# Kernel optimization log

Measured on AMD Instinct MI355X. Metric: run time of the kernel, lower is better.

## Reference

```python
import jax, jax.numpy as jnp
import numpy as np

B, N, D, H = 4, 256, 32, 512

def setup_inputs() -> dict:
    key = jax.random.key(0)
    ks = jax.random.split(key, 6)
    z = jax.random.normal(ks[0], (B, N, D), dtype=jnp.float32)
    motif_mask = (jax.random.uniform(ks[1], (B, N)) > 0.5).astype(jnp.float32)
    residue_mask = jnp.ones((B, N), dtype=jnp.float32)
    # Linear weights stored as (in, out); scaled like torch default init
    W1 = jax.random.normal(ks[2], (D * D, H), dtype=jnp.float32) / np.sqrt(D * D)
    b1 = jnp.zeros((H,), dtype=jnp.float32)
    W2 = jax.random.normal(ks[3], (H, H // 2), dtype=jnp.float32) / np.sqrt(H)
    b2 = jnp.zeros((H // 2,), dtype=jnp.float32)
    W3 = jax.random.normal(ks[4], (H // 2, 1), dtype=jnp.float32) / np.sqrt(H // 2)
    b3 = jnp.zeros((1,), dtype=jnp.float32)
    return {"z": z, "motif_mask": motif_mask, "residue_mask": residue_mask,
            "W1": W1, "b1": b1, "W2": W2, "b2": b2, "W3": W3, "b3": b3}

def reference(z, motif_mask, residue_mask, W1, b1, W2, b2, W3, b3):
    # kron[b,i,j, a*D+c] = z[b,i,a] * z[b,j,c]; first Linear on kron is the
    # bilinear form z_i^T W1_h z_j -- compute via two matmuls, never
    # materializing the (B,N,N,D^2) tensor.
    d = z.shape[-1]
    W1r = W1.reshape(d, d, -1)                      # (D, D, H); axis0 = z_i dim, axis1 = z_j dim
    tmp = jnp.einsum('bia,ach->bihc', z, W1r)        # (B, N, H, D)
    h1 = jax.nn.relu(jnp.einsum('bihc,bjc->bijh', tmp, z) + b1)  # (B, N, N, H)
    h2 = jax.nn.relu(jnp.einsum('bijh,hk->bijk', h1, W2) + b2)   # (B, N, N, H/2)
    contact_logits = (jnp.einsum('bijk,ko->bijo', h2, W3) + b3)[..., 0]  # (B, N, N)
    outer_mask = motif_mask[:, None, :] * motif_mask[:, :, None]
    contact_logits = contact_logits * outer_mask
    contact_map = jax.nn.sigmoid(contact_logits)
    return (contact_map, contact_logits)
```

## Files before the change

### kernel.cpp

```cpp
#include <hip/hip_runtime.h>
#include <hip/hip_bf16.h>
#include <cstdint>
#include <cstddef>

#define NB 4
#define NN 256
#define DD 32
#define HH 512

typedef __attribute__((ext_vector_type(8))) short short8;
typedef __attribute__((ext_vector_type(4))) float f32x4;
typedef __attribute__((ext_vector_type(16))) float f32x16;

static __device__ __forceinline__ unsigned cvtpk(float a, float b) {
  unsigned r;
  asm("v_cvt_pk_bf16_f32 %0, %1, %2" : "=v"(r) : "v"(a), "v"(b));
  return r;
}
static __device__ __forceinline__ unsigned short f2bf1(float a) {
  return (unsigned short)(cvtpk(a, 0.f) & 0xffffu);
}

static __device__ __forceinline__ short8 pack8(float4 a0, float4 a1) {
  union { unsigned u[4]; short8 s; } r;
  r.u[0] = cvtpk(a0.x, a0.y); r.u[1] = cvtpk(a0.z, a0.w);
  r.u[2] = cvtpk(a1.x, a1.y); r.u[3] = cvtpk(a1.z, a1.w);
  return r.s;
}

__global__ __launch_bounds__(256) void prep0(const float* __restrict__ W1,
                                             unsigned short* __restrict__ W1F) {
  const int f = blockIdx.x * 256 + threadIdx.x;
  #pragma unroll
  for (int r = 0; r < 4; ++r) {
    int row = r * 16384 + f;
    int lane = row & 63;
    int nt = (row >> 6) & 7, w2 = (row >> 9) & 3, nblk = row >> 11;
    int quad = lane >> 4, l16 = lane & 15;
    int nl = w2 * 128 + l16 * 8 + nt;
    int hl = nl >> 5, c = nl & 31;
    const float* src = W1 + (size_t)(nblk * 16 + hl);
    float v[8];
    #pragma unroll
    for (int e = 0; e < 8; ++e)
      v[e] = src[(size_t)((quad * 8 + e) * 32 + c) * 512];
    uint4 p;
    p.x = cvtpk(v[0], v[1]); p.y = cvtpk(v[2], v[3]);
    p.z = cvtpk(v[4], v[5]); p.w = cvtpk(v[6], v[7]);
    *(uint4*)&W1F[(size_t)row * 8] = p;
  }
}

__global__ __launch_bounds__(256) void prep1(const float* __restrict__ z,
                                             const unsigned short* __restrict__ W1F,
                                             const float* __restrict__ W2,
                                             const float* __restrict__ motif,
                                             unsigned short* __restrict__ W2F,
                                             unsigned short* __restrict__ Tall,
                                             int* __restrict__ jlist,
                                             int* __restrict__ jcnt,
                                             int* __restrict__ wq,
                                             int* __restrict__ wqn,
                                             float* __restrict__ out) {
  const int blk = blockIdx.x;
  const int tid = threadIdx.x;
  if (blk < 512) {
    const int nblk = blk >> 4, mgrp = blk & 15;
    const int bibase = mgrp * 64;
    const int w2 = tid >> 6, lane = tid & 63;
    const int quad = lane >> 4, l16 = lane & 15;

    short8 bfr[8];
    #pragma unroll
    for (int nt = 0; nt < 8; ++nt)
      bfr[nt] = *(const short8*)&W1F[(size_t)((((nblk * 4 + w2) * 8) + nt) * 64 + lane) * 8];

    const int ncol = nblk * 512 + w2 * 128 + l16 * 8;
    #pragma unroll
    for (int mtg = 0; mtg < 2; ++mtg) {
      short8 afr[2];
      #pragma unroll
      for (int mi = 0; mi < 2; ++mi) {
        const float* zr = z + (size_t)(bibase + (mtg * 2 + mi) * 16 + l16) * 32 + quad * 8;
        float4 a0 = *(const float4*)(zr);
        float4 a1 = *(const float4*)(zr + 4);
        afr[mi] = pack8(a0, a1);
      }
      f32x4 d[2][8];
      #pragma unroll
      for (int mi = 0; mi < 2; ++mi)
        #pragma unroll
        for (int nt = 0; nt < 8; ++nt)
          d[mi][nt] = __builtin_amdgcn_mfma_f32_16x16x32_bf16(
              afr[mi], bfr[nt], (f32x4){0.f, 0.f, 0.f, 0.f}, 0, 0, 0);
      #pragma unroll
      for (int mi = 0; mi < 2; ++mi)
        #pragma unroll
        for (int r = 0; r < 4; ++r) {
          int rowbi = bibase + (mtg * 2 + mi) * 16 + quad * 4 + r;
          if (motif[rowbi] != 0.f) {
            uint4 p;
            p.x = cvtpk(d[mi][0][r], d[mi][1][r]);
            p.y = cvtpk(d[mi][2][r], d[mi][3][r]);
            p.z = cvtpk(d[mi][4][r], d[mi][5][r]);
            p.w = cvtpk(d[mi][6][r], d[mi][7][r]);
            *(uint4*)&Tall[(size_t)rowbi * 16384 + ncol] = p;
          }
        }
    }
  } else if (blk < 576) {
    int f8 = (blk - 512) * 256 + tid;
    int lane = f8 & 63;
    int nt = (f8 >> 6) & 1, s = (f8 >> 7) & 3, hc = (f8 >> 9) & 7, w = (f8 >> 12) & 3;
    int k2 = w * 64 + nt * 32 + (lane & 31);
    int hb = hc * 64 + s * 16 + (lane >> 5) * 8;
    float v[8];
    #pragma unroll
    for (int e = 0; e < 8; ++e) v[e] = W2[(hb + e) * 256 + k2];
    uint4 p;
    p.x = cvtpk(v[0], v[1]); p.y = cvtpk(v[2], v[3]);
    p.z = cvtpk(v[4], v[5]); p.w = cvtpk(v[6], v[7]);
    ((uint4*)W2F)[f8] = p;
  } else if (blk == 576) {
    __shared__ int itemc[4];
    __shared__ int baseh[4];
    const int w = tid >> 6, lane = tid & 63;
    int cnt = 0;
    if (w < NB) {
      #pragma unroll
      for (int ch = 0; ch < 4; ++ch) {
        int j = ch * 64 + lane;
        float m = motif[w * 256 + j];
        bool alive = (m != 0.f);
        unsigned long long mk = __ballot(alive);
        unsigned long long below = mk & ((1ull << lane) - 1ull);
        int pos = __popcll(below);
        if (alive) jlist[w * 256 + cnt + pos] = j;
        cnt += __popcll(mk);
      }
      if (lane == 0) {
        jcnt[w] = cnt;
        itemc[w] = cnt * ((cnt + 63) >> 6);
      }
    }
    __syncthreads();
    if (tid == 0) {
      int s = 0;
      #pragma unroll
      for (int k = 0; k < NB; ++k) { baseh[k] = s; s += itemc[k]; }
      *wqn = s;
    }
    __syncthreads();
    if (w < NB) {
      const int K = (cnt + 63) >> 6;
      const int base = baseh[w];
      const int L2n = cnt * K;
      int rank = 0;
      #pragma unroll
      for (int ch = 0; ch < 4; ++ch) {
        int i = ch * 64 + lane;
        bool alive = (motif[w * 256 + i] != 0.f);
        unsigned long long mk = __ballot(alive);
        unsigned long long below = mk & ((1ull << lane) - 1ull);
        int pos = __popcll(below);
        if (alive) {
          int idx0 = (rank + pos) * K;
          for (int jt = 0; jt < K; ++jt) {
            int idx = idx0 + jt;
            int nidx = idx;
            if (K == 2) {
              int g = idx >> 4;
              if (g * 16 + 16 <= L2n)
                nidx = g * 16 + ((idx & 1) << 3) + ((idx >> 1) & 7);
            }
            wq[base + nidx] = (w * 256 + i) * 4 + jt;
          }
        }
        rank += __popcll(mk);
      }
    }
  } else {
    const size_t OUT2 = (size_t)NB * NN * NN;
    const int c = blk - 577;
    for (int p = c * 4096 + tid; p < (c + 1) * 4096; p += 256) {
      int bi = p >> 8, j = p & 255, b = bi >> 8;
      if (motif[bi] == 0.f || motif[b * 256 + j] == 0.f) {
        out[p] = 0.5f;
        out[OUT2 + p] = 0.f;
      }
    }
  }
}

__global__ __launch_bounds__(256, 4) void fused(const unsigned short* __restrict__ Tall,
                                             const unsigned short* __restrict__ W2F,
                                             const float* __restrict__ z,
                                             const float* __restrict__ b1,
                                             const float* __restrict__ b2,
                                             const float* __restrict__ W3,
                                             const float* __restrict__ b3,
                                             const float* __restrict__ motif,
                                             const int* __restrict__ jlist,
                                             const int* __restrict__ jcnt,
                                             const int* __restrict__ wq,
                                             const int* __restrict__ wqn,
                                             float* __restrict__ out) {
  __shared__ unsigned short h1s[64 * 264];
  __shared__ float red[2][256];

  const int bx = blockIdx.x;
  const int tid = threadIdx.x;
  const size_t OUT2 = (size_t)NB * NN * NN;
  const int nq = *wqn;

  if (bx >= nq) return;
  const int item = wq[bx];

  const int w = tid >> 6, lane = tid & 63;
  const int quad = lane >> 4, l16 = lane & 15;
  const int L = lane >> 5, c32 = lane & 31;

  const int bi = item >> 2, jt = item & 3;
  const int b = bi >> 8;
  const int cnt = jcnt[b];
  const int slotbase = jt * 64;
  const float mi_v = motif[bi];

  short8 zfr[4];
  #pragma unroll
  for (int sg = 0; sg < 4; ++sg) {
    int slot = slotbase + sg * 16 + l16;
    int sc = slot < cnt ? slot : cnt - 1;
    int jj = jlist[b * 256 + sc] & 255;
    const float* zr = z + (size_t)(b * 256 + jj) * 32 + quad * 8;
    float4 a0 = *(const float4*)(zr);
    float4 a1 = *(const float4*)(zr + 4);
    zfr[sg] = pack8(a0, a1);
  }

  const unsigned short* Tbase = Tall + (size_t)bi * 16384 + (w * 16 + l16) * 32 + quad * 8;
  const unsigned short* Wp = W2F + w * 32768 + lane * 8;
  const float* b1base = b1 + w * 16 + quad * 4;

  #pragma unroll 1
  for (int nt = 0; nt < 2; ++nt) {
    const int k2 = w * 64 + nt * 32 + c32;
    const float b2s = b2[k2];
    const float w3s = W3[k2];

    f32x16 acc[2];
    acc[0] = (f32x16){0.f,0.f,0.f,0.f,0.f,0.f,0.f,0.f,
                      0.f,0.f,0.f,0.f,0.f,0.f,0.f,0.f};
    acc[1] = acc[0];

    #pragma unroll 1
    for (int half = 0; half < 2; ++half) {
      short8 tfr[4];
      #pragma unroll
      for (int q = 0; q < 4; ++q)
        tfr[q] = *(const short8*)(Tbase + (half * 4 + q) * 2048);
      #pragma unroll
      for (int q = 0; q < 4; ++q) {
        float4 b1f = *(const float4*)(b1base + (half * 4 + q) * 64);
        f32x4 cin = {b1f.x, b1f.y, b1f.z, b1f.w};
        #pragma unroll
        for (int sg = 0; sg < 4; ++sg) {
          f32x4 d = __builtin_amdgcn_mfma_f32_16x16x32_bf16(
              tfr[q], zfr[sg], cin, 0, 0, 0);
          uint2 p;
          p.x = cvtpk(fmaxf(d[0], 0.f), fmaxf(d[1], 0.f));
          p.y = cvtpk(fmaxf(d[2], 0.f), fmaxf(d[3], 0.f));
          *(uint2*)&h1s[(sg * 16 + l16) * 264 + q * 64 + w * 16 + quad * 4] = p;
        }
      }
      __syncthreads();

      const unsigned short* Wh = Wp + half * 16384 + nt * 512;
      const unsigned short* h1r = &h1s[c32 * 264 + L * 8];
      short8 bfp[3], afp[2][2];
      #pragma unroll
      for (int p = 0; p < 3; ++p)
        bfp[p] = *(const short8*)(Wh + p * 1024);
      afp[0][0] = *(const short8*)(h1r);
      afp[0][1] = *(const short8*)(h1r + 32 * 264);
      afp[1][0] = *(const short8*)(h1r + 16);
      afp[1][1] = *(const short8*)(h1r + 32 * 264 + 16);
      #pragma unroll
      for (int u = 0; u < 16; ++u) {
        const int cur = u & 1, bq = u % 3;
        short8 a0 = afp[cur][0], a1 = afp[cur][1];
        short8 b0 = bfp[bq];
        if (u < 14) {
          afp[cur][0] = *(const short8*)(h1r + (u + 2) * 16);
          afp[cur][1] = *(const short8*)(h1r + 32 * 264 + (u + 2) * 16);
        }
        if (u < 13)
          bfp[bq] = *(const short8*)(Wh + (u + 3) * 1024);
        acc[0] = __builtin_amdgcn_mfma_f32_32x32x16_bf16(a0, b0, acc[0], 0, 0, 0);
        acc[1] = __builtin_amdgcn_mfma_f32_32x32x16_bf16(a1, b0, acc[1], 0, 0, 0);
      }

      if (half == 1) {
        float pr[2][16];
        #pragma unroll
        for (int mt = 0; mt < 2; ++mt)
          #pragma unroll
          for (int reg = 0; reg < 16; ++reg) {
            float v = acc[mt][reg] + b2s;
            v = v > 0.f ? v : 0.f;
            float s = v * w3s;
            s += __shfl_xor(s, 1);
            s += __shfl_xor(s, 2);
            s += __shfl_xor(s, 4);
            s += __shfl_xor(s, 8);
            s += __shfl_xor(s, 16);
            pr[mt][reg] = s;
          }
        if (c32 == 0) {
          #pragma unroll
          for (int mt = 0; mt < 2; ++mt)
            #pragma unroll
            for (int g = 0; g < 4; ++g) {
              float4 vv = {pr[mt][g * 4 + 0], pr[mt][g * 4 + 1],
                           pr[mt][g * 4 + 2], pr[mt][g * 4 + 3]};
              *(float4*)&red[nt][w * 64 + mt * 32 + g * 8 + L * 4] = vv;
            }
        }
      }
      __syncthreads();
    }
  }

  if (tid < 64) {
    int slot = slotbase + tid;
    if (slot < cnt) {
      int j = jlist[b * 256 + slot] & 255;
      float logit = b3[0];
      #pragma unroll
      for (int wv = 0; wv < 4; ++wv)
        logit += red[0][wv * 64 + tid] + red[1][wv * 64 + tid];
      float mm = mi_v * motif[b * 256 + j];
      logit *= mm;
      float map = 1.f / (1.f + expf(-logit));
      size_t idx = (size_t)bi * 256 + j;
      out[idx] = map;
      out[OUT2 + idx] = logit;
    }
  }
}

extern "C" void kernel_launch(void* const* d_in, const int* in_sizes, int n_in,
                              void* d_out, int out_size, void* d_ws, size_t ws_size,
                              hipStream_t stream) {
  const float* z     = (const float*)d_in[0];
  const float* motif = (const float*)d_in[1];
  const float* W1 = (const float*)d_in[3];
  const float* b1 = (const float*)d_in[4];
  const float* W2 = (const float*)d_in[5];
  const float* b2 = (const float*)d_in[6];
  const float* W3 = (const float*)d_in[7];
  const float* b3 = (const float*)d_in[8];
  float* out = (float*)d_out;

  char* ws = (char*)d_ws;
  unsigned short* Tall = (unsigned short*)ws;
  unsigned short* W2F  = (unsigned short*)(ws + 33554432);
  unsigned short* W1F  = (unsigned short*)(ws + 33554432 + 262144);
  char* tail = ws + 33554432 + 262144 + 1048576;
  int* jlist = (int*)(tail);
  int* jcnt  = (int*)(tail + 4096);
  int* wq    = (int*)(tail + 4096 + 64);
  int* wqn   = (int*)(tail + 4096 + 64 + 16384);

  prep0<<<64, 256, 0, stream>>>(W1, W1F);
  prep1<<<641, 256, 0, stream>>>(z, W1F, W2, motif, W2F, Tall,
                                 jlist, jcnt, wq, wqn, out);
  fused<<<4096, 256, 0, stream>>>(Tall, W2F, z, b1, b2, W3, b3, motif,
                                  jlist, jcnt, wq, wqn, out);
}
```

Measured before the change: 135.6 us.

## Use 512-thread blocks so each wave owns one output-column tile in fused kernel

Doubles the fused kernel's block size to 8 waves. Each wave now computes one 32-wide slice of the second-layer output instead of looping over two. The first-layer h1 computation is split between wave pairs, and the outer nt loop is removed, so h1 is computed once per block instead of twice. The trade-off is lower occupancy per block and different register pressure under the relaxed launch bounds, which may affect latency hiding.

```diff
diff --git a/kernel.cpp b/kernel.cpp
--- a/kernel.cpp
+++ b/kernel.cpp
@@ -192,7 +192,7 @@
   }
 }
 
-__global__ __launch_bounds__(256, 4) void fused(const unsigned short* __restrict__ Tall,
+__global__ __launch_bounds__(512) void fused(const unsigned short* __restrict__ Tall,
                                              const unsigned short* __restrict__ W2F,
                                              const float* __restrict__ z,
                                              const float* __restrict__ b1,
@@ -206,7 +206,7 @@
                                              const int* __restrict__ wqn,
                                              float* __restrict__ out) {
   __shared__ unsigned short h1s[64 * 264];
-  __shared__ float red[2][256];
+  __shared__ float red[512];
 
   const int bx = blockIdx.x;
   const int tid = threadIdx.x;
@@ -219,6 +219,8 @@
   const int w = tid >> 6, lane = tid & 63;
   const int quad = lane >> 4, l16 = lane & 15;
   const int L = lane >> 5, c32 = lane & 31;
+  const int wcol = w & 3;
+  const int sgh = w >> 2;
 
   const int bi = item >> 2, jt = item & 3;
   const int b = bi >> 8;
@@ -226,119 +228,113 @@
   const int slotbase = jt * 64;
   const float mi_v = motif[bi];
 
-  short8 zfr[4];
+  short8 zfr[2];
   #pragma unroll
-  for (int sg = 0; sg < 4; ++sg) {
-    int slot = slotbase + sg * 16 + l16;
+  for (int sgl = 0; sgl < 2; ++sgl) {
+    int slot = slotbase + (sgh * 2 + sgl) * 16 + l16;
     int sc = slot < cnt ? slot : cnt - 1;
     int jj = jlist[b * 256 + sc] & 255;
     const float* zr = z + (size_t)(b * 256 + jj) * 32 + quad * 8;
     float4 a0 = *(const float4*)(zr);
     float4 a1 = *(const float4*)(zr + 4);
-    zfr[sg] = pack8(a0, a1);
-  }
-
-  const unsigned short* Tbase = Tall + (size_t)bi * 16384 + (w * 16 + l16) * 32 + quad * 8;
-  const unsigned short* Wp = W2F + w * 32768 + lane * 8;
-  const float* b1base = b1 + w * 16 + quad * 4;
+    zfr[sgl] = pack8(a0, a1);
+  }
+
+  const int k2 = w * 32 + c32;
+  const float b2s = b2[k2];
+  const float w3s = W3[k2];
+
+  f32x16 acc[2];
+  acc[0] = (f32x16){0.f,0.f,0.f,0.f,0.f,0.f,0.f,0.f,
+                    0.f,0.f,0.f,0.f,0.f,0.f,0.f,0.f};
+  acc[1] = acc[0];
+
+  const unsigned short* Tbase = Tall + (size_t)bi * 16384 + (wcol * 16 + l16) * 32 + quad * 8;
+  const unsigned short* Wp = W2F + (w >> 1) * 32768 + (w & 1) * 512 + lane * 8;
+  const float* b1base = b1 + wcol * 16 + quad * 4;
 
   #pragma unroll 1
-  for (int nt = 0; nt < 2; ++nt) {
-    const int k2 = w * 64 + nt * 32 + c32;
-    const float b2s = b2[k2];
-    const float w3s = W3[k2];
-
-    f32x16 acc[2];
-    acc[0] = (f32x16){0.f,0.f,0.f,0.f,0.f,0.f,0.f,0.f,
-                      0.f,0.f,0.f,0.f,0.f,0.f,0.f,0.f};
-    acc[1] = acc[0];
-
-    #pragma unroll 1
-    for (int half = 0; half < 2; ++half) {
-      short8 tfr[4];
-      #pragma unroll
-      for (int q = 0; q < 4; ++q)
-        tfr[q] = *(const short8*)(Tbase + (half * 4 + q) * 2048);
-      #pragma unroll
-      for (int q = 0; q < 4; ++q) {
-        float4 b1f = *(const float4*)(b1base + (half * 4 + q) * 64);
-        f32x4 cin = {b1f.x, b1f.y, b1f.z, b1f.w};
-        #pragma unroll
-        for (int sg = 0; sg < 4; ++sg) {
-          f32x4 d = __builtin_amdgcn_mfma_f32_16x16x32_bf16(
-              tfr[q], zfr[sg], cin, 0, 0, 0);
-          uint2 p;
-          p.x = cvtpk(fmaxf(d[0], 0.f), fmaxf(d[1], 0.f));
-          p.y = cvtpk(fmaxf(d[2], 0.f), fmaxf(d[3], 0.f));
-          *(uint2*)&h1s[(sg * 16 + l16) * 264 + q * 64 + w * 16 + quad * 4] = p;
-        }
-      }
-      __syncthreads();
-
-      const unsigned short* Wh = Wp + half * 16384 + nt * 512;
-      const unsigned short* h1r = &h1s[c32 * 264 + L * 8];
-      short8 bfp[3], afp[2][2];
-      #pragma unroll
-      for (int p = 0; p < 3; ++p)
-        bfp[p] = *(const short8*)(Wh + p * 1024);
-      afp[0][0] = *(const short8*)(h1r);
-      afp[0][1] = *(const short8*)(h1r + 32 * 264);
-      afp[1][0] = *(const short8*)(h1r + 16);
-      afp[1][1] = *(const short8*)(h1r + 32 * 264 + 16);
-      #pragma unroll
-      for (int u = 0; u < 16; ++u) {
-        const int cur = u & 1, bq = u % 3;
-        short8 a0 = afp[cur][0], a1 = afp[cur][1];
-        short8 b0 = bfp[bq];
-        if (u < 14) {
-          afp[cur][0] = *(const short8*)(h1r + (u + 2) * 16);
-          afp[cur][1] = *(const short8*)(h1r + 32 * 264 + (u + 2) * 16);
-        }
-        if (u < 13)
-          bfp[bq] = *(const short8*)(Wh + (u + 3) * 1024);
-        acc[0] = __builtin_amdgcn_mfma_f32_32x32x16_bf16(a0, b0, acc[0], 0, 0, 0);
-        acc[1] = __builtin_amdgcn_mfma_f32_32x32x16_bf16(a1, b0, acc[1], 0, 0, 0);
-      }
-
-      if (half == 1) {
-        float pr[2][16];
-        #pragma unroll
-        for (int mt = 0; mt < 2; ++mt)
-          #pragma unroll
-          for (int reg = 0; reg < 16; ++reg) {
-            float v = acc[mt][reg] + b2s;
-            v = v > 0.f ? v : 0.f;
-            float s = v * w3s;
-            s += __shfl_xor(s, 1);
-            s += __shfl_xor(s, 2);
-            s += __shfl_xor(s, 4);
-            s += __shfl_xor(s, 8);
-            s += __shfl_xor(s, 16);
-            pr[mt][reg] = s;
-          }
-        if (c32 == 0) {
-          #pragma unroll
-          for (int mt = 0; mt < 2; ++mt)
-            #pragma unroll
-            for (int g = 0; g < 4; ++g) {
-              float4 vv = {pr[mt][g * 4 + 0], pr[mt][g * 4 + 1],
-                           pr[mt][g * 4 + 2], pr[mt][g * 4 + 3]};
-              *(float4*)&red[nt][w * 64 + mt * 32 + g * 8 + L * 4] = vv;
-            }
-        }
-      }
-      __syncthreads();
-    }
-  }
-
+  for (int half = 0; half < 2; ++half) {
+    short8 tfr[4];
+    #pragma unroll
+    for (int q = 0; q < 4; ++q)
+      tfr[q] = *(const short8*)(Tbase + (half * 4 + q) * 2048);
+    #pragma unroll
+    for (int q = 0; q < 4; ++q) {
+      float4 b1f = *(const float4*)(b1base + (half * 4 + q) * 64);
+      f32x4 cin = {b1f.x, b1f.y, b1f.z, b1f.w};
+      #pragma unroll
+      for (int sgl = 0; sgl < 2; ++sgl) {
+        f32x4 d = __builtin_amdgcn_mfma_f32_16x16x32_bf16(
+            tfr[q], zfr[sgl], cin, 0, 0, 0);
+        uint2 p;
+        p.x = cvtpk(fmaxf(d[0], 0.f), fmaxf(d[1], 0.f));
+        p.y = cvtpk(fmaxf(d[2], 0.f), fmaxf(d[3], 0.f));
+        *(uint2*)&h1s[((sgh * 2 + sgl) * 16 + l16) * 264 + q * 64 + wcol * 16 + quad * 4] = p;
+      }
+    }
+    __syncthreads();
+
+    const unsigned short* Wh = Wp + half * 16384;
+    const unsigned short* h1r = &h1s[c32 * 264 + L * 8];
+    short8 bfp[3], afp[2][2];
+    #pragma unroll
+    for (int p = 0; p < 3; ++p)
+      bfp[p] = *(const short8*)(Wh + p * 1024);
+    afp[0][0] = *(const short8*)(h1r);
+    afp[0][1] = *(const short8*)(h1r + 32 * 264);
+    afp[1][0] = *(const short8*)(h1r + 16);
+    afp[1][1] = *(const short8*)(h1r + 32 * 264 + 16);
+    #pragma unroll
+    for (int u = 0; u < 16; ++u) {
+      const int cur = u & 1, bq = u % 3;
+      short8 a0 = afp[cur][0], a1 = afp[cur][1];
+      short8 b0 = bfp[bq];
+      if (u < 14) {
+        afp[cur][0] = *(const short8*)(h1r + (u + 2) * 16);
+        afp[cur][1] = *(const short8*)(h1r + 32 * 264 + (u + 2) * 16);
+      }
+      if (u < 13)
+        bfp[bq] = *(const short8*)(Wh + (u + 3) * 1024);
+      acc[0] = __builtin_amdgcn_mfma_f32_32x32x16_bf16(a0, b0, acc[0], 0, 0, 0);
+      acc[1] = __builtin_amdgcn_mfma_f32_32x32x16_bf16(a1, b0, acc[1], 0, 0, 0);
+    }
+    if (half == 0) __syncthreads();
+  }
+
+  float pr[2][16];
+  #pragma unroll
+  for (int mt = 0; mt < 2; ++mt)
+    #pragma unroll
+    for (int reg = 0; reg < 16; ++reg) {
+      float v = acc[mt][reg] + b2s;
+      v = v > 0.f ? v : 0.f;
+      float s = v * w3s;
+      s += __shfl_xor(s, 1);
+      s += __shfl_xor(s, 2);
+      s += __shfl_xor(s, 4);
+      s += __shfl_xor(s, 8);
+      s += __shfl_xor(s, 16);
+      pr[mt][reg] = s;
+    }
+  if (c32 == 0) {
+    #pragma unroll
+    for (int mt = 0; mt < 2; ++mt)
+      #pragma unroll
+      for (int g = 0; g < 4; ++g) {
+        float4 vv = {pr[mt][g * 4 + 0], pr[mt][g * 4 + 1],
+                     pr[mt][g * 4 + 2], pr[mt][g * 4 + 3]};
+        *(float4*)&red[w * 64 + mt * 32 + g * 8 + L * 4] = vv;
+      }
+  }
+  __syncthreads();
   if (tid < 64) {
     int slot = slotbase + tid;
     if (slot < cnt) {
       int j = jlist[b * 256 + slot] & 255;
       float logit = b3[0];
       #pragma unroll
-      for (int wv = 0; wv < 4; ++wv)
-        logit += red[0][wv * 64 + tid] + red[1][wv * 64 + tid];
+      for (int wv = 0; wv < 8; ++wv) logit += red[wv * 64 + tid];
       float mm = mi_v * motif[b * 256 + j];
       logit *= mm;
       float map = 1.f / (1.f + expf(-logit));
@@ -375,6 +371,6 @@
   prep0<<<64, 256, 0, stream>>>(W1, W1F);
   prep1<<<641, 256, 0, stream>>>(z, W1F, W2, motif, W2F, Tall,
                                  jlist, jcnt, wq, wqn, out);
-  fused<<<4096, 256, 0, stream>>>(Tall, W2F, z, b1, b2, W3, b3, motif,
+  fused<<<4096, 512, 0, stream>>>(Tall, W2F, z, b1, b2, W3, b3, motif,
                                   jlist, jcnt, wq, wqn, out);
 }
```

Result: faster. 130.0 us (-4.1%).
